# Kernel tuning notes

Measured on AMD Instinct MI355X. Metric: run time of the kernel, lower is better.

Reference implementation:

```python
import jax, jax.numpy as jnp
import numpy as np

C, D, B = 32768, 1024, 16384
LABEL = 0.95  # EMA keep factor from __init__ default


def setup_inputs() -> dict:
    key = jax.random.key(0)
    k1, k2, k3, k4 = jax.random.split(key, 4)
    return {
        "s_logits": jax.random.normal(k1, (C, D), dtype=jnp.float32),
        "t_logits": jax.random.normal(k2, (C, D), dtype=jnp.float32),
        "logits": jax.random.normal(k3, (B, D), dtype=jnp.float32),
        "the_class": jax.random.randint(k4, (B,), 0, C, dtype=jnp.int64),
    }


def _ema_scatter(table, logits, the_class, keep):
    """Sequential per-row EMA: for i in range(B): table[c_i] = table[c_i]*keep + logits[i]*(1-keep).
    Vectorized: row c with k occurrences -> table[c]*keep^k + (1-keep)*sum_j keep^{#later occurrences} * logits[j].
    """
    Bn = the_class.shape[0]
    Cn = table.shape[0]
    dt = table.dtype
    ones = jnp.ones((Bn,), dtype=dt)
    counts = jax.ops.segment_sum(ones, the_class, num_segments=Cn)  # [C]
    # occurrence rank (0-based, in original batch order) of each sample within its class
    order = jnp.argsort(the_class)  # stable sort preserves batch order within a class
    sc = the_class[order]
    first = jnp.searchsorted(sc, sc, side="left")  # start of each class segment
    rank_sorted = jnp.arange(Bn, dtype=jnp.int32) - first.astype(jnp.int32)
    rank = jnp.zeros((Bn,), jnp.int32).at[order].set(rank_sorted)
    # number of later same-class occurrences
    r = counts[the_class] - 1.0 - rank.astype(dt)  # [B]
    w = (1.0 - keep) * jnp.power(jnp.asarray(keep, dt), r)  # [B]
    contrib = jax.ops.segment_sum(logits * w[:, None], the_class, num_segments=Cn)  # [C, D]
    decay = jnp.power(jnp.asarray(keep, dt), counts)  # [C]; rows absent from batch keep decay=1
    return table * decay[:, None] + contrib


def reference(s_logits, t_logits, logits, the_class):
    new_s = _ema_scatter(s_logits, logits, the_class, LABEL)  # update(type='s')
    loss = jnp.mean(jnp.sum(jnp.abs(new_s - t_logits), axis=1))  # loss()
    return loss
```

## Files before the change

kernel.cpp:

```cpp
#include <hip/hip_runtime.h>

#define NC 32768
#define ND 1024
#define NQ 256
#define NB 16384
#define KEEP 0.95f
#define OMK  0.05f
#define KCAP 16
#define RPB 8

__global__ void count_scatter_kernel(const int* __restrict__ the_class,
                                     int* __restrict__ counts,
                                     int* __restrict__ idx_list) {
    int i = blockIdx.x * blockDim.x + threadIdx.x;
    if (i < NB) {
        int c = the_class[i];
        int pos = atomicAdd(&counts[c], 1);
        if (pos < KCAP) idx_list[c * KCAP + pos] = i;
    }
}

__global__ void wprep_kernel(const int* __restrict__ counts,
                             const int* __restrict__ idx_list,
                             float* __restrict__ decays,
                             int2* __restrict__ elist) {
    int c = blockIdx.x * blockDim.x + threadIdx.x;
    int cnt = counts[c];
    float base = KEEP, r = 1.0f;
    for (int e = cnt; e > 0; e >>= 1) { if (e & 1) r *= base; base *= base; }
    decays[c] = r;
    int m = cnt < KCAP ? cnt : KCAP;
    int idx[KCAP];
    for (int j = 0; j < m; ++j) idx[j] = idx_list[c * KCAP + j];
    for (int j = 0; j < m; ++j) {
        int later = 0;
        for (int l = 0; l < m; ++l) later += (idx[l] > idx[j]);
        float w = OMK;
        for (int k = 0; k < later; ++k) w *= KEEP;
        int2 e; e.x = idx[j]; e.y = __float_as_int(w);
        elist[c * KCAP + j] = e;
    }
}

__global__ __launch_bounds__(256) void loss_kernel(
    const float* __restrict__ s_logits,
    const float* __restrict__ t_logits,
    const float* __restrict__ logits,
    const int*   __restrict__ counts,
    const float* __restrict__ decays,
    const int2*  __restrict__ elist,
    float* __restrict__ out) {

    const int q  = threadIdx.x;
    const int c0 = blockIdx.x * RPB;

    const float4* s4 = (const float4*)s_logits;
    const float4* t4 = (const float4*)t_logits;
    const float4* l4 = (const float4*)logits;

    float4 sv[RPB], tv[RPB];
    #pragma unroll
    for (int r = 0; r < RPB; ++r) sv[r] = s4[(size_t)(c0 + r) * NQ + q];
    #pragma unroll
    for (int r = 0; r < RPB; ++r) tv[r] = t4[(size_t)(c0 + r) * NQ + q];

    float dec[RPB]; int m[RPB];
    #pragma unroll
    for (int r = 0; r < RPB; ++r) {
        dec[r] = decays[c0 + r];
        int cnt = counts[c0 + r];
        m[r] = cnt < KCAP ? cnt : KCAP;
    }

    float lsum = 0.0f;
    #pragma unroll
    for (int r = 0; r < RPB; ++r) {
        const int c = c0 + r;
        float4 acc;
        acc.x = sv[r].x * dec[r];
        acc.y = sv[r].y * dec[r];
        acc.z = sv[r].z * dec[r];
        acc.w = sv[r].w * dec[r];
        for (int j = 0; j < m[r]; ++j) {
            int2 e = elist[c * KCAP + j];
            const float w = __int_as_float(e.y);
            float4 lv = l4[(size_t)e.x * NQ + q];
            acc.x = fmaf(w, lv.x, acc.x);
            acc.y = fmaf(w, lv.y, acc.y);
            acc.z = fmaf(w, lv.z, acc.z);
            acc.w = fmaf(w, lv.w, acc.w);
        }
        lsum += fabsf(acc.x - tv[r].x) + fabsf(acc.y - tv[r].y) +
                fabsf(acc.z - tv[r].z) + fabsf(acc.w - tv[r].w);
    }

    #pragma unroll
    for (int off = 32; off > 0; off >>= 1) lsum += __shfl_down(lsum, off);
    __shared__ float wsum[4];
    const int wave = threadIdx.x >> 6, lane = threadIdx.x & 63;
    if (lane == 0) wsum[wave] = lsum;
    __syncthreads();
    if (threadIdx.x == 0) {
        float total = (wsum[0] + wsum[1] + wsum[2] + wsum[3]) * (1.0f / NC);
        atomicAdd(out, total);
    }
}

extern "C" void kernel_launch(void* const* d_in, const int* in_sizes, int n_in,
                              void* d_out, int out_size, void* d_ws, size_t ws_size,
                              hipStream_t stream) {
    const float* s_logits  = (const float*)d_in[0];
    const float* t_logits  = (const float*)d_in[1];
    const float* logits    = (const float*)d_in[2];
    const int*   the_class = (const int*)d_in[3];
    float* out = (float*)d_out;

    int*   counts   = (int*)d_ws;
    int*   idx_list = counts + NC;
    float* decays   = (float*)(idx_list + NC * KCAP);
    int2*  elist    = (int2*)(decays + NC);

    hipMemsetAsync(counts, 0, NC * sizeof(int), stream);
    hipMemsetAsync(d_out, 0, sizeof(float), stream);

    count_scatter_kernel<<<NB / 256, 256, 0, stream>>>(the_class, counts, idx_list);
    wprep_kernel<<<NC / 256, 256, 0, stream>>>(counts, idx_list, decays, elist);
    loss_kernel<<<NC / RPB, 256, 0, stream>>>(s_logits, t_logits, logits,
                                              counts, decays, elist, out);
}
```

Baseline: 335.9 us.

## Prefetch first two gathered logits rows per class with padded entry list

The entry list is padded with zero-weight entries so the loss kernel can unconditionally issue gather loads for the first two entries of each class up front. These loads are in flight alongside the s/t row loads, instead of being issued serially inside a data-dependent loop. The s/t streams now use nontemporal loads, and rows per block drop from 8 to 4. In exchange, wprep writes every padded entry slot, and classes with zero or one entry do wasted gathers of row 0.

```diff
diff --git a/kernel.cpp b/kernel.cpp
--- a/kernel.cpp
+++ b/kernel.cpp
@@ -7,7 +7,10 @@
 #define KEEP 0.95f
 #define OMK  0.05f
 #define KCAP 16
-#define RPB 8
+#define JPAD 2
+#define RPB  4
+
+typedef float fx4 __attribute__((ext_vector_type(4)));
 
 __global__ void count_scatter_kernel(const int* __restrict__ the_class,
                                      int* __restrict__ counts,
@@ -32,12 +35,17 @@
     int m = cnt < KCAP ? cnt : KCAP;
     int idx[KCAP];
     for (int j = 0; j < m; ++j) idx[j] = idx_list[c * KCAP + j];
-    for (int j = 0; j < m; ++j) {
-        int later = 0;
-        for (int l = 0; l < m; ++l) later += (idx[l] > idx[j]);
-        float w = OMK;
-        for (int k = 0; k < later; ++k) w *= KEEP;
-        int2 e; e.x = idx[j]; e.y = __float_as_int(w);
+    for (int j = 0; j < KCAP; ++j) {
+        int2 e;
+        if (j < m) {
+            int later = 0;
+            for (int l = 0; l < m; ++l) later += (idx[l] > idx[j]);
+            float w = OMK;
+            for (int k = 0; k < later; ++k) w *= KEEP;
+            e.x = idx[j]; e.y = __float_as_int(w);
+        } else {
+            e.x = 0; e.y = __float_as_int(0.0f);
+        }
         elist[c * KCAP + j] = e;
     }
 }
@@ -54,41 +62,56 @@
     const int q  = threadIdx.x;
     const int c0 = blockIdx.x * RPB;
 
-    const float4* s4 = (const float4*)s_logits;
-    const float4* t4 = (const float4*)t_logits;
-    const float4* l4 = (const float4*)logits;
+    const fx4* s4 = (const fx4*)s_logits;
+    const fx4* t4 = (const fx4*)t_logits;
+    const fx4* l4 = (const fx4*)logits;
 
-    float4 sv[RPB], tv[RPB];
-    #pragma unroll
-    for (int r = 0; r < RPB; ++r) sv[r] = s4[(size_t)(c0 + r) * NQ + q];
-    #pragma unroll
-    for (int r = 0; r < RPB; ++r) tv[r] = t4[(size_t)(c0 + r) * NQ + q];
-
-    float dec[RPB]; int m[RPB];
+    float dec[RPB]; int m[RPB]; int2 ge[RPB][JPAD];
     #pragma unroll
     for (int r = 0; r < RPB; ++r) {
         dec[r] = decays[c0 + r];
         int cnt = counts[c0 + r];
         m[r] = cnt < KCAP ? cnt : KCAP;
+        #pragma unroll
+        for (int j = 0; j < JPAD; ++j) ge[r][j] = elist[(c0 + r) * KCAP + j];
+    }
+
+    fx4 sv[RPB], tv[RPB], gv[RPB][JPAD];
+    #pragma unroll
+    for (int r = 0; r < RPB; ++r)
+        sv[r] = __builtin_nontemporal_load(&s4[(size_t)(c0 + r) * NQ + q]);
+    #pragma unroll
+    for (int r = 0; r < RPB; ++r)
+        tv[r] = __builtin_nontemporal_load(&t4[(size_t)(c0 + r) * NQ + q]);
+    #pragma unroll
+    for (int r = 0; r < RPB; ++r) {
+        #pragma unroll
+        for (int j = 0; j < JPAD; ++j)
+            gv[r][j] = l4[(size_t)ge[r][j].x * NQ + q];
     }
 
     float lsum = 0.0f;
     #pragma unroll
     for (int r = 0; r < RPB; ++r) {
-        const int c = c0 + r;
-        float4 acc;
-        acc.x = sv[r].x * dec[r];
-        acc.y = sv[r].y * dec[r];
-        acc.z = sv[r].z * dec[r];
-        acc.w = sv[r].w * dec[r];
-        for (int j = 0; j < m[r]; ++j) {
-            int2 e = elist[c * KCAP + j];
-            const float w = __int_as_float(e.y);
-            float4 lv = l4[(size_t)e.x * NQ + q];
-            acc.x = fmaf(w, lv.x, acc.x);
-            acc.y = fmaf(w, lv.y, acc.y);
-            acc.z = fmaf(w, lv.z, acc.z);
-            acc.w = fmaf(w, lv.w, acc.w);
+        fx4 acc = sv[r] * dec[r];
+        #pragma unroll
+        for (int j = 0; j < JPAD; ++j) {
+            const float w = __int_as_float(ge[r][j].y);
+            acc.x = fmaf(w, gv[r][j].x, acc.x);
+            acc.y = fmaf(w, gv[r][j].y, acc.y);
+            acc.z = fmaf(w, gv[r][j].z, acc.z);
+            acc.w = fmaf(w, gv[r][j].w, acc.w);
+        }
+        if (m[r] > JPAD) {
+            for (int j = JPAD; j < m[r]; ++j) {
+                int2 e = elist[(c0 + r) * KCAP + j];
+                const float w = __int_as_float(e.y);
+                fx4 lv = l4[(size_t)e.x * NQ + q];
+                acc.x = fmaf(w, lv.x, acc.x);
+                acc.y = fmaf(w, lv.y, acc.y);
+                acc.z = fmaf(w, lv.z, acc.z);
+                acc.w = fmaf(w, lv.w, acc.w);
+            }
         }
         lsum += fabsf(acc.x - tv[r].x) + fabsf(acc.y - tv[r].y) +
                 fabsf(acc.z - tv[r].z) + fabsf(acc.w - tv[r].w);
@@ -120,8 +143,8 @@
     float* decays   = (float*)(idx_list + NC * KCAP);
     int2*  elist    = (int2*)(decays + NC);
 
-    hipMemsetAsync(counts, 0, NC * sizeof(int), stream);
-    hipMemsetAsync(d_out, 0, sizeof(float), stream);
+    (void)hipMemsetAsync(counts, 0, NC * sizeof(int), stream);
+    (void)hipMemsetAsync(d_out, 0, sizeof(float), stream);
 
     count_scatter_kernel<<<NB / 256, 256, 0, stream>>>(the_class, counts, idx_list);
     wprep_kernel<<<NC / 256, 256, 0, stream>>>(counts, idx_list, decays, elist);
```

Result: slower. 358.2 us (+6.6%).
